# Kernel optimization log

Hardware: AMD Instinct MI355X
Metric: run time of the kernel (lower is better)

Reference implementation:

```python
import jax, jax.numpy as jnp
import numpy as np

B, T, C, HS = 4, 4096, 1024, 128

def setup_inputs() -> dict:
    key = jax.random.key(0)
    kx, kk, kq, kv = jax.random.split(key, 4)
    x = jax.random.normal(kx, (B, T, C), dtype=jnp.float32)
    # torch Linear(n_embd, head_size, bias=False): y = x @ W.T with W [hs, C].
    # We store the transposed form W [C, hs] so y = x @ W (same math).
    s = C ** -0.5  # kaiming-ish scale to keep activations sane
    Wk = jax.random.normal(kk, (C, HS), dtype=jnp.float32) * s
    Wq = jax.random.normal(kq, (C, HS), dtype=jnp.float32) * s
    Wv = jax.random.normal(kv, (C, HS), dtype=jnp.float32) * s
    return {"x": x, "Wk": Wk, "Wq": Wq, "Wv": Wv}

def reference(x, Wk, Wq, Wv):
    # Single causal self-attention head (dropout = identity, eval mode).
    k = jnp.einsum('btc,ch->bth', x, Wk)  # [B,T,hs]
    q = jnp.einsum('btc,ch->bth', x, Wq)
    v = jnp.einsum('btc,ch->bth', x, Wv)
    scale = k.shape[-1] ** -0.5
    wei = jnp.einsum('bqh,bkh->bqk', q, k) * scale  # [B,T,T]
    Tq = x.shape[1]
    causal = jnp.tril(jnp.ones((Tq, Tq), dtype=bool))
    wei = jnp.where(causal, wei, -jnp.inf)
    wei = jax.nn.softmax(wei, axis=-1)
    out = jnp.einsum('bqk,bkh->bqh', wei, v)  # [B,T,hs]
    return out
```

## Files before the change

### kernel.cpp

```cpp
#include <hip/hip_runtime.h>
#include <hip/hip_bf16.h>
#include <math.h>

#define B_  4
#define T_  4096
#define C_  1024
#define HS_ 128

using bf16x8 = __attribute__((ext_vector_type(8))) __bf16;
using bf16x4 = __attribute__((ext_vector_type(4))) __bf16;
using f32x4  = __attribute__((ext_vector_type(4))) float;

#define MFMA(a, b, c) __builtin_amdgcn_mfma_f32_16x16x32_bf16(a, b, c, 0, 0, 0)

typedef __attribute__((address_space(1))) const float gfloat;
typedef __attribute__((address_space(3))) float lfloat;

__device__ inline float fexp2(float x) {
  float r;
  asm volatile("v_exp_f32 %0, %1\n\ts_nop 0" : "=v"(r) : "v"(x));
  return r;
}


__global__ __launch_bounds__(256) void prep_w_kernel(
    const float* __restrict__ Wk, const float* __restrict__ Wq,
    const float* __restrict__ Wv, __bf16* __restrict__ Wf) {
  const int m  = blockIdx.x >> 4;
  const int k0 = (blockIdx.x & 15) * 64;
  const float* W = (m == 0) ? Wq : ((m == 1) ? Wk : Wv);
  const float scale = (m == 0) ? (0.08838834764831845f * 1.4426950408889634f) : 1.0f;
  __shared__ __bf16 tile[128][72];
  const int t = threadIdx.x;
#pragma unroll
  for (int p = 0; p < 8; ++p) {
    int e  = p * 1024 + t * 4;
    int r  = e >> 7;
    int cc = e & 127;
    float4 w = *reinterpret_cast<const float4*>(&W[(size_t)(k0 + r) * HS_ + cc]);
    tile[cc + 0][r] = (__bf16)(w.x * scale);
    tile[cc + 1][r] = (__bf16)(w.y * scale);
    tile[cc + 2][r] = (__bf16)(w.z * scale);
    tile[cc + 3][r] = (__bf16)(w.w * scale);
  }
  __syncthreads();
#pragma unroll
  for (int p = 0; p < 4; ++p) {
    int e  = p * 2048 + t * 8;
    int n  = e >> 6;
    int kk = e & 63;
    bf16x8 v;
#pragma unroll
    for (int jj = 0; jj < 8; ++jj) v[jj] = tile[n][kk + jj];
    int u  = m * 8 + (n >> 4);
    int ts = (k0 + kk) >> 5;
    int g2 = (kk >> 3) & 3;
    *reinterpret_cast<bf16x8*>(
        &Wf[((size_t)(u * 32 + ts) * 64 + g2 * 16 + (n & 15)) * 8]) = v;
  }
}

__device__ inline bf16x8 cvt8p(float4 u, float4 v) {
  bf16x8 r;
  r[0] = (__bf16)u.x; r[1] = (__bf16)u.y; r[2] = (__bf16)u.z; r[3] = (__bf16)u.w;
  r[4] = (__bf16)v.x; r[5] = (__bf16)v.y; r[6] = (__bf16)v.z; r[7] = (__bf16)v.w;
  return r;
}

__global__ __launch_bounds__(512) void proj_kernel(
    const float* __restrict__ x, const __bf16* __restrict__ Wf,
    __bf16* __restrict__ Qf, __bf16* __restrict__ Kf, __bf16* __restrict__ Vf) {
  __shared__ __align__(16) char lds[61440];
  const int tid = threadIdx.x;
  const int wid = tid >> 6;
  const int l   = tid & 63;
  const int c   = l & 15;
  const int g   = l >> 4;
  const int rbase = blockIdx.x * 32;

  f32x4 acc[3][2];
#pragma unroll
  for (int i = 0; i < 3; ++i) { acc[i][0] = 0.f; acc[i][1] = 0.f; }

  const float* xsrc[2];
#pragma unroll
  for (int op = 0; op < 2; ++op) {
    int id  = op * 512 + tid;
    int row = id >> 5;
    int w   = id & 31;
    int sf  = ((((w >> 2) ^ (row & 7)) << 2) | (w & 3));
    xsrc[op] = x + (size_t)(rbase + row) * C_ + sf;
  }
  const __bf16* wsrc[3];
  int wdst[3];
#pragma unroll
  for (int i = 0; i < 3; ++i) {
    int id = i * 512 + tid;
    int u  = id >> 6;
    int ln = id & 63;
    wsrc[i] = Wf + (size_t)u * 32 * 512 + ln * 8;
    wdst[i] = id * 16;
  }

  auto xstage = [&](int t, int xbo) {
#pragma unroll
    for (int op = 0; op < 2; ++op)
      __builtin_amdgcn_global_load_lds((gfloat*)(xsrc[op] + t * 32),
          (lfloat*)(lds + xbo + (op * 512 + tid) * 4), 4, 0, 0);
  };
  auto wstage = [&](int t, int wbo) {
#pragma unroll
    for (int i = 0; i < 3; ++i)
      __builtin_amdgcn_global_load_lds((gfloat*)(wsrc[i] + t * 512),
          (lfloat*)(lds + wbo + wdst[i]), 16, 0, 0);
  };

  int woffs[3];
#pragma unroll
  for (int i = 0; i < 3; ++i)
    woffs[i] = (wid * 3 + i) * 1024 + l * 16;
  int xoffs[2][2];
#pragma unroll
  for (int rt = 0; rt < 2; ++rt) {
    int row = rt * 16 + c;
#pragma unroll
    for (int j = 0; j < 2; ++j)
      xoffs[rt][j] = row * 128 + ((((g << 1) | j) ^ (row & 7)) << 4);
  }

  xstage(0, 0);
  wstage(0, 12288);
  xstage(1, 4096);
  asm volatile("s_waitcnt vmcnt(2)" ::: "memory");
  __syncthreads();

  int xb_cur = 0, xb_nxt = 4096, xb_fut = 8192;
  for (int t = 0; t < 32; ++t) {
    const int wbo = 12288 + (t & 1) * 24576;
    if (t + 1 < 32) wstage(t + 1, 12288 + ((t + 1) & 1) * 24576);
    const bool more2 = (t + 2 < 32);
    if (more2) xstage(t + 2, xb_fut);

    bf16x8 wf[3];
#pragma unroll
    for (int i = 0; i < 3; ++i)
      wf[i] = *reinterpret_cast<const bf16x8*>(lds + wbo + woffs[i]);
#pragma unroll
    for (int rt = 0; rt < 2; ++rt) {
      float4 lo = *reinterpret_cast<const float4*>(lds + xb_cur + xoffs[rt][0]);
      float4 hi = *reinterpret_cast<const float4*>(lds + xb_cur + xoffs[rt][1]);
      bf16x8 a = cvt8p(lo, hi);
#pragma unroll
      for (int i = 0; i < 3; ++i) acc[i][rt] = MFMA(a, wf[i], acc[i][rt]);
    }

    if (more2) {
      asm volatile("s_waitcnt vmcnt(2)" ::: "memory");
    } else {
      asm volatile("s_waitcnt vmcnt(0)" ::: "memory");
    }
    __syncthreads();
    int tmp = xb_cur; xb_cur = xb_nxt; xb_nxt = xb_fut; xb_fut = tmp;
  }

  const size_t tile = blockIdx.x;
#pragma unroll
  for (int i = 0; i < 3; ++i) {
    const int u = wid * 3 + i;
    const int m = u >> 3, nt = u & 7;
    const int gprime = ((nt & 1) << 1) + (c >> 3);
    const int e = c & 7;
    if (m == 0) {
#pragma unroll
      for (int rt = 0; rt < 2; ++rt)
#pragma unroll
        for (int rr = 0; rr < 4; ++rr)
          Qf[(tile * 8 + rt * 4 + (nt >> 1)) * 512 +
             (gprime * 16 + 4 * g + rr) * 8 + e] = (__bf16)acc[i][rt][rr];
    } else if (m == 1) {
#pragma unroll
      for (int rt = 0; rt < 2; ++rt)
#pragma unroll
        for (int rr = 0; rr < 4; ++rr)
          Kf[(tile * 8 + 2 * (nt >> 1) + (g & 1)) * 512 +
             (gprime * 16 + (((2 * rt + (g >> 1)) << 2) | rr)) * 8 + e] =
              (__bf16)acc[i][rt][rr];
    } else {
#pragma unroll
      for (int rt = 0; rt < 2; ++rt) {
        bf16x4 v4;
#pragma unroll
        for (int rr = 0; rr < 4; ++rr) v4[rr] = (__bf16)acc[i][rt][rr];
        *reinterpret_cast<bf16x4*>(
            Vf + (tile * 8 + nt) * 512 +
            ((2 * rt + (g >> 1)) * 16 + c) * 8 + 4 * (g & 1)) = v4;
      }
    }
  }
}

__global__ __launch_bounds__(256, 2) void attn_kernel(
    const __bf16* __restrict__ Qf, const __bf16* __restrict__ Kf,
    const __bf16* __restrict__ Vf, float* __restrict__ out) {
  __shared__ float sm[4][32];
  __shared__ float sl[4][32];
  __shared__ float bufA[32][132];
  __shared__ float bufB[32][132];

  const int tid = threadIdx.x;
  const int wid = tid >> 6;
  const int l   = tid & 63;
  const int c   = l & 15;
  const int g   = l >> 4;
  const int bid = blockIdx.x;
  const int b   = (bid & 7) >> 1;
  const int j   = ((bid >> 3) << 1) | (bid & 1);
  const int qt  = (j < 64) ? (127 - j) : (j - 64);
  const int qb  = qt * 32;

  bf16x8 qf[2][4];
  {
    const __bf16* Qt = Qf + (size_t)(b * 128 + qt) * 4096 + l * 8;
#pragma unroll
    for (int rt = 0; rt < 2; ++rt)
#pragma unroll
      for (int cs = 0; cs < 4; ++cs)
        qf[rt][cs] = *reinterpret_cast<const bf16x8*>(Qt + (rt * 4 + cs) * 512);
  }

  f32x4 acc[2][8];
#pragma unroll
  for (int i = 0; i < 2; ++i)
#pragma unroll
    for (int d = 0; d < 8; ++d) acc[i][d] = 0.f;
  float mrun[2] = {-INFINITY, -INFINITY};
  float lrun[2] = {0.f, 0.f};

  if (wid <= qt) {
    const __bf16* Kb8 = Kf + (size_t)b * 128 * 4096 + l * 8;
    const __bf16* Vb8 = Vf + (size_t)b * 128 * 4096 + l * 8;
    bf16x8 kreg[8];
    auto kload = [&](int kt) {
      const __bf16* kb = Kb8 + (size_t)kt * 4096;
#pragma unroll
      for (int jj = 0; jj < 8; ++jj)
        kreg[jj] = *reinterpret_cast<const bf16x8*>(kb + jj * 512);
    };
    kload(wid);

    for (int kt = wid; kt <= qt; kt += 4) {
      f32x4 s00 = 0.f, s01 = 0.f, s10 = 0.f, s11 = 0.f;
      __builtin_amdgcn_s_setprio(1);
#pragma unroll
      for (int cs = 0; cs < 4; ++cs) {
        s00 = MFMA(kreg[2 * cs], qf[0][cs], s00);
        s01 = MFMA(kreg[2 * cs + 1], qf[0][cs], s01);
        s10 = MFMA(kreg[2 * cs], qf[1][cs], s10);
        s11 = MFMA(kreg[2 * cs + 1], qf[1][cs], s11);
      }
      __builtin_amdgcn_s_setprio(0);

      bf16x8 vf[8];
      {
        const __bf16* vb = Vb8 + (size_t)kt * 4096;
#pragma unroll
        for (int db = 0; db < 8; ++db)
          vf[db] = *reinterpret_cast<const bf16x8*>(vb + db * 512);
      }

      if (kt + 4 <= qt) kload(kt + 4);

      const bool maskt = (kt == qt);
      bf16x8 pb[2];
#pragma unroll
      for (int rt = 0; rt < 2; ++rt) {
        float p[8];
        const f32x4 sa = rt ? s10 : s00;
        const f32x4 sb = rt ? s11 : s01;
#pragma unroll
        for (int rr = 0; rr < 4; ++rr) { p[rr] = sa[rr]; p[4 + rr] = sb[rr]; }
        if (maskt) {
          const int lim = rt * 16 + c;
#pragma unroll
          for (int jj = 0; jj < 8; ++jj)
            if (8 * g + jj > lim) p[jj] = -INFINITY;
        }
        float t0 = fmaxf(fmaxf(p[0], p[1]), p[2]);
        float t1 = fmaxf(fmaxf(p[3], p[4]), p[5]);
        float t2 = fmaxf(fmaxf(p[6], p[7]), t0);
        float tmax = fmaxf(t1, t2);

        if (!__all(tmax <= mrun[rt] + 11.5415603f)) {
          float cmax = fmaxf(tmax, __shfl_xor(tmax, 16));
          cmax = fmaxf(cmax, __shfl_xor(cmax, 32));
          float mnew = fmaxf(mrun[rt], cmax);
          float al   = fexp2(mrun[rt] - mnew);
          mrun[rt] = mnew;
          lrun[rt] *= al;
#pragma unroll
          for (int db = 0; db < 8; ++db) acc[rt][db] *= al;
        }
        const float mc = mrun[rt];
#pragma unroll
        for (int jj = 0; jj < 8; ++jj) p[jj] = fexp2(p[jj] - mc);
        lrun[rt] += ((p[0] + p[1]) + (p[2] + p[3])) + ((p[4] + p[5]) + (p[6] + p[7]));
#pragma unroll
        for (int jj = 0; jj < 8; ++jj) pb[rt][jj] = (__bf16)p[jj];
      }

      __builtin_amdgcn_s_setprio(1);
#pragma unroll
      for (int db = 0; db < 8; ++db) {
        acc[0][db] = MFMA(vf[db], pb[0], acc[0][db]);
        acc[1][db] = MFMA(vf[db], pb[1], acc[1][db]);
      }
      __builtin_amdgcn_s_setprio(0);
    }
  }

#pragma unroll
  for (int rt = 0; rt < 2; ++rt) {
    lrun[rt] += __shfl_xor(lrun[rt], 16);
    lrun[rt] += __shfl_xor(lrun[rt], 32);
  }

  if (g == 0) {
    sm[wid][c] = mrun[0]; sm[wid][16 + c] = mrun[1];
    sl[wid][c] = lrun[0]; sl[wid][16 + c] = lrun[1];
  }
  __syncthreads();

  float linv[2];
#pragma unroll
  for (int rt = 0; rt < 2; ++rt) {
    const int q = rt * 16 + c;
    float ms = fmaxf(fmaxf(sm[0][q], sm[1][q]), fmaxf(sm[2][q], sm[3][q]));
    float ls = fexp2(sm[0][q] - ms) * sl[0][q] + fexp2(sm[1][q] - ms) * sl[1][q]
             + fexp2(sm[2][q] - ms) * sl[2][q] + fexp2(sm[3][q] - ms) * sl[3][q];
    float al = fexp2(mrun[rt] - ms);
#pragma unroll
    for (int db = 0; db < 8; ++db) acc[rt][db] *= al;
    linv[rt] = 1.0f / ls;
  }

  auto store_buf = [&](float(*buf)[132]) {
#pragma unroll
    for (int rt = 0; rt < 2; ++rt)
#pragma unroll
      for (int db = 0; db < 8; ++db)
        *reinterpret_cast<f32x4*>(&buf[rt * 16 + c][db * 16 + 4 * g]) = acc[rt][db];
  };
  auto add_buf = [&](float(*buf)[132]) {
#pragma unroll
    for (int rt = 0; rt < 2; ++rt)
#pragma unroll
      for (int db = 0; db < 8; ++db)
        acc[rt][db] += *reinterpret_cast<const f32x4*>(&buf[rt * 16 + c][db * 16 + 4 * g]);
  };

  if (wid == 2) store_buf(bufA);
  if (wid == 3) store_buf(bufB);
  __syncthreads();
  if (wid == 0) add_buf(bufA);
  if (wid == 1) add_buf(bufB);
  __syncthreads();
  if (wid == 1) store_buf(bufA);
  __syncthreads();
  if (wid == 0) {
    add_buf(bufA);
    float* op = out + ((size_t)b * T_ + qb) * HS_;
#pragma unroll
    for (int rt = 0; rt < 2; ++rt)
#pragma unroll
      for (int db = 0; db < 8; ++db) {
        f32x4 v = acc[rt][db] * linv[rt];
        *reinterpret_cast<f32x4*>(op + (size_t)(rt * 16 + c) * HS_ + db * 16 + 4 * g) = v;
      }
  }
}

extern "C" void kernel_launch(void* const* d_in, const int* in_sizes, int n_in,
                              void* d_out, int out_size, void* d_ws, size_t ws_size,
                              hipStream_t stream) {
  const float* x  = (const float*)d_in[0];
  const float* Wk = (const float*)d_in[1];
  const float* Wq = (const float*)d_in[2];
  const float* Wv = (const float*)d_in[3];
  float* out = (float*)d_out;

  char* ws = (char*)d_ws;
  __bf16* Wf = (__bf16*)ws;
  __bf16* Qf = (__bf16*)(ws + 786432);
  __bf16* Kf = (__bf16*)(ws + 786432 + 4194304);
  __bf16* Vf = (__bf16*)(ws + 786432 + 8388608);

  prep_w_kernel<<<48, 256, 0, stream>>>(Wk, Wq, Wv, Wf);
  proj_kernel<<<512, 512, 0, stream>>>(x, Wf, Qf, Kf, Vf);
  attn_kernel<<<512, 256, 0, stream>>>(Qf, Kf, Vf, out);
}
```

Before: 65.05 us.

## Load projection weights directly into registers instead of staging through LDS

In the projection kernel, each wave now reads its bf16 weight fragments straight from global memory into registers, replacing the double-buffered LDS staging. LDS shrinks from 60 KB to 12 KB, which is meant to allow more resident blocks and to drop the LDS write/read round trip for data no other wave reuses. The explicit vmcnt waits are replaced by a bare s_barrier. This relies on in-order completion of vector memory ops, and on the compiler's waits for the weight registers, to make the async x tiles in LDS visible. Weight loads are now exposed latency inside the loop, with no prefetch distance.

After: 63.86 us. No clear change (-1.8%).

```diff
diff --git a/kernel.cpp b/kernel.cpp
--- a/kernel.cpp
+++ b/kernel.cpp
@@ -70,7 +70,7 @@
 __global__ __launch_bounds__(512) void proj_kernel(
     const float* __restrict__ x, const __bf16* __restrict__ Wf,
     __bf16* __restrict__ Qf, __bf16* __restrict__ Kf, __bf16* __restrict__ Vf) {
-  __shared__ __align__(16) char lds[61440];
+  __shared__ __align__(16) char lds[12288];
   const int tid = threadIdx.x;
   const int wid = tid >> 6;
   const int l   = tid & 63;
@@ -91,34 +91,15 @@
     int sf  = ((((w >> 2) ^ (row & 7)) << 2) | (w & 3));
     xsrc[op] = x + (size_t)(rbase + row) * C_ + sf;
   }
-  const __bf16* wsrc[3];
-  int wdst[3];
-#pragma unroll
-  for (int i = 0; i < 3; ++i) {
-    int id = i * 512 + tid;
-    int u  = id >> 6;
-    int ln = id & 63;
-    wsrc[i] = Wf + (size_t)u * 32 * 512 + ln * 8;
-    wdst[i] = id * 16;
-  }
-
   auto xstage = [&](int t, int xbo) {
 #pragma unroll
     for (int op = 0; op < 2; ++op)
       __builtin_amdgcn_global_load_lds((gfloat*)(xsrc[op] + t * 32),
           (lfloat*)(lds + xbo + (op * 512 + tid) * 4), 4, 0, 0);
   };
-  auto wstage = [&](int t, int wbo) {
-#pragma unroll
-    for (int i = 0; i < 3; ++i)
-      __builtin_amdgcn_global_load_lds((gfloat*)(wsrc[i] + t * 512),
-          (lfloat*)(lds + wbo + wdst[i]), 16, 0, 0);
-  };
-
-  int woffs[3];
-#pragma unroll
-  for (int i = 0; i < 3; ++i)
-    woffs[i] = (wid * 3 + i) * 1024 + l * 16;
+
+  const __bf16* wb = Wf + (size_t)(wid * 3) * 16384 + l * 8;
+
   int xoffs[2][2];
 #pragma unroll
   for (int rt = 0; rt < 2; ++rt) {
@@ -129,22 +110,19 @@
   }
 
   xstage(0, 0);
-  wstage(0, 12288);
   xstage(1, 4096);
   asm volatile("s_waitcnt vmcnt(2)" ::: "memory");
-  __syncthreads();
+  __builtin_amdgcn_s_barrier();
 
   int xb_cur = 0, xb_nxt = 4096, xb_fut = 8192;
   for (int t = 0; t < 32; ++t) {
-    const int wbo = 12288 + (t & 1) * 24576;
-    if (t + 1 < 32) wstage(t + 1, 12288 + ((t + 1) & 1) * 24576);
-    const bool more2 = (t + 2 < 32);
-    if (more2) xstage(t + 2, xb_fut);
-
     bf16x8 wf[3];
 #pragma unroll
     for (int i = 0; i < 3; ++i)
-      wf[i] = *reinterpret_cast<const bf16x8*>(lds + wbo + woffs[i]);
+      wf[i] = *reinterpret_cast<const bf16x8*>(wb + i * 16384 + t * 512);
+
+    if (t + 2 < 32) xstage(t + 2, xb_fut);
+
 #pragma unroll
     for (int rt = 0; rt < 2; ++rt) {
       float4 lo = *reinterpret_cast<const float4*>(lds + xb_cur + xoffs[rt][0]);
@@ -154,12 +132,9 @@
       for (int i = 0; i < 3; ++i) acc[i][rt] = MFMA(a, wf[i], acc[i][rt]);
     }
 
-    if (more2) {
-      asm volatile("s_waitcnt vmcnt(2)" ::: "memory");
-    } else {
-      asm volatile("s_waitcnt vmcnt(0)" ::: "memory");
-    }
-    __syncthreads();
+    asm volatile("" ::: "memory");
+    __builtin_amdgcn_s_barrier();
+    asm volatile("" ::: "memory");
     int tmp = xb_cur; xb_cur = xb_nxt; xb_nxt = xb_fut; xb_fut = tmp;
   }
 
```
